# Kernel optimization log

Hardware: AMD Instinct MI355X
Metric: run time of the kernel (lower is better)

Reference implementation:

```python
import jax, jax.numpy as jnp
import numpy as np

D_M, D_K, D_V, HEADS = 1024, 64, 64, 16
B, S = 2, 2048


def setup_inputs() -> dict:
    key = jax.random.key(0)
    ks = jax.random.split(key, 5)
    x = jax.random.normal(ks[0], (B, S, D_M), dtype=jnp.float32)
    # per-head projection weights (original deep-copies one rand init per head;
    # we give each head independent weights, matching the per-head param structure)
    Wk = jax.random.uniform(ks[1], (HEADS, D_M, D_K), dtype=jnp.float32)
    Wq = jax.random.uniform(ks[2], (HEADS, D_M, D_K), dtype=jnp.float32)
    Wv = jax.random.uniform(ks[3], (HEADS, D_M, D_V), dtype=jnp.float32)
    Wo = jax.random.uniform(ks[4], (HEADS * D_V, D_M), dtype=jnp.float32)
    return {"x": x, "Wk": Wk, "Wq": Wq, "Wv": Wv, "Wo": Wo}


def reference(x, Wk, Wq, Wv, Wo):
    # per-head QKV projections, batched over heads: [B,H,S,d]
    q = jnp.einsum("bsm,hmk->bhsk", x, Wq)
    k = jnp.einsum("bsm,hmk->bhsk", x, Wk)
    v = jnp.einsum("bsm,hmv->bhsv", x, Wv)
    scale = 1.0 / jnp.sqrt(jnp.asarray(q.shape[-1], dtype=q.dtype))
    scores = jnp.einsum("bhsk,bhtk->bhst", q, k) * scale  # [B,H,S,S]
    attn = jax.nn.softmax(scores, axis=-1)
    ctx = jnp.einsum("bhst,bhtv->bhsv", attn, v)  # [B,H,S,d_v]
    # concat heads -> [B,S,H*d_v], then output projection
    ctx = jnp.transpose(ctx, (0, 2, 1, 3)).reshape(x.shape[0], x.shape[1], -1)
    return jnp.einsum("bsc,cm->bsm", ctx, Wo)
```

## Files before the change

### kernel.cpp

```cpp
#include <hip/hip_runtime.h>
#include <hip/hip_bf16.h>
#include <stdint.h>

#define DM   1024
#define DKV  64
#define HEADS 16
#define BATCH 2
#define SEQ  2048
#define BS   (BATCH*SEQ)
#define BHD  (BATCH*HEADS)

typedef __attribute__((ext_vector_type(8))) short bf16x8;
typedef __attribute__((ext_vector_type(4))) short bf16x4;
typedef __attribute__((ext_vector_type(4))) float f32x4;

__device__ inline unsigned short bf16_rtn(float f) {
  union { float f; unsigned u; } v; v.f = f;
  unsigned u = v.u;
  unsigned r = u + 0x7fffu + ((u >> 16) & 1u);
  return (unsigned short)(r >> 16);
}
__device__ inline float bf16_to_f(unsigned short h) {
  union { unsigned u; float f; } v; v.u = ((unsigned)h) << 16; return v.f;
}
__device__ inline void split_bf16(float x, unsigned short& hi, unsigned short& lo) {
  hi = bf16_rtn(x);
  lo = bf16_rtn(x - bf16_to_f(hi));
}

__device__ inline float fast_exp2(float x) {
#if __has_builtin(__builtin_amdgcn_exp2f)
  return __builtin_amdgcn_exp2f(x);
#else
  return exp2f(x);
#endif
}

__device__ inline f32x4 mfma16x16x16_bf16(bf16x4 a, bf16x4 b, f32x4 c) {
#if __has_builtin(__builtin_amdgcn_mfma_f32_16x16x16bf16_1k)
  return __builtin_amdgcn_mfma_f32_16x16x16bf16_1k(a, b, c, 0, 0, 0);
#else
  asm volatile("v_mfma_f32_16x16x16_bf16 %0, %1, %2, %0" : "+v"(c) : "v"(a), "v"(b));
  return c;
#endif
}

__device__ inline void stage16(const unsigned short* g, unsigned short* lds_base, int lane) {
#if __has_builtin(__builtin_amdgcn_global_load_lds)
  __builtin_amdgcn_global_load_lds((__attribute__((address_space(1))) void*)(g),
                                   (__attribute__((address_space(3))) void*)(lds_base),
                                   16, 0, 0);
#else
  *(bf16x8*)(lds_base + lane * 8) = *(const bf16x8*)g;
#endif
}

__global__ void cvt_x_split(const float* __restrict__ x,
                            unsigned short* __restrict__ xh, unsigned short* __restrict__ xl) {
  int i = (blockIdx.x * 256 + threadIdx.x) * 8;
  bf16x8 oh, ol;
  #pragma unroll
  for (int j = 0; j < 8; ++j) {
    unsigned short hi, lo;
    split_bf16(x[i + j], hi, lo);
    oh[j] = (short)hi; ol[j] = (short)lo;
  }
  *(bf16x8*)(xh + i) = oh;
  *(bf16x8*)(xl + i) = ol;
}

__global__ void pack_qkv_split(const float* __restrict__ Wq, const float* __restrict__ Wk,
                               const float* __restrict__ Wv,
                               unsigned short* __restrict__ Wh, unsigned short* __restrict__ Wl) {
  __shared__ float tile[64][65];
  int bid = blockIdx.x;
  int p = bid >> 8, h = (bid >> 4) & 15, mt = bid & 15;
  const float* W = (p == 0) ? Wq : (p == 1) ? Wk : Wv;
  const float* src = W + (size_t)h * (DM * DKV);
  int t = threadIdx.x;
  int m0 = mt * 64;
  #pragma unroll
  for (int pass = 0; pass < 16; ++pass) {
    int row = pass * 4 + (t >> 6), col = t & 63;
    tile[row][col] = src[(size_t)(m0 + row) * DKV + col];
  }
  __syncthreads();
  int cbase = p * 1024 + h * 64;
  #pragma unroll
  for (int pass = 0; pass < 16; ++pass) {
    int krow = pass * 4 + (t >> 6), mcol = t & 63;
    unsigned short hi, lo;
    split_bf16(tile[mcol][krow], hi, lo);
    size_t idx = (size_t)(cbase + krow) * DM + m0 + mcol;
    Wh[idx] = hi; Wl[idx] = lo;
  }
}

__global__ void pack_wo(const float* __restrict__ Wo, unsigned short* __restrict__ WoT) {
  __shared__ float tile[64][65];
  int ib = blockIdx.x >> 4, jb = blockIdx.x & 15;
  int t = threadIdx.x;
  #pragma unroll
  for (int pass = 0; pass < 16; ++pass) {
    int row = pass * 4 + (t >> 6), col = t & 63;
    tile[row][col] = Wo[(size_t)(ib * 64 + row) * DM + jb * 64 + col];
  }
  __syncthreads();
  #pragma unroll
  for (int pass = 0; pass < 16; ++pass) {
    int a = pass * 4 + (t >> 6), b = t & 63;
    WoT[(size_t)(jb * 64 + a) * DM + ib * 64 + b] = bf16_rtn(tile[b][a]);
  }
}

__global__ __launch_bounds__(256, 2)
void gemm1_split(const unsigned short* __restrict__ Ah, const unsigned short* __restrict__ Al,
                 const unsigned short* __restrict__ Bh, const unsigned short* __restrict__ Bl,
                 unsigned short* __restrict__ Qh, unsigned short* __restrict__ Ql,
                 unsigned short* __restrict__ Kh, unsigned short* __restrict__ Kl,
                 unsigned short* __restrict__ Vt) {
  __shared__ unsigned short AsH[128 * 32], AsL[128 * 32];
  __shared__ unsigned short BsH[128 * 32], BsL[128 * 32];
  const int tid = threadIdx.x;
  const int w = tid >> 6, lane = tid & 63;
  const int quad = lane >> 4, l16 = lane & 15;
  const int wm = w >> 1, wn = w & 1;
  const int bm = blockIdx.x, bn = blockIdx.y;

  f32x4 acc[4][4];
  #pragma unroll
  for (int i = 0; i < 4; ++i)
    #pragma unroll
    for (int j = 0; j < 4; ++j) acc[i][j] = (f32x4){0.f, 0.f, 0.f, 0.f};

  const int r4 = lane >> 2, c4 = lane & 3;
  const size_t offA = (size_t)(bm * 128 + w * 32 + r4) * DM + c4 * 8;
  const size_t offB = (size_t)(bn * 128 + w * 32 + r4) * DM + c4 * 8;
  unsigned short* lAh0 = AsH + (w * 32) * 32;      unsigned short* lAh1 = AsH + (w * 32 + 16) * 32;
  unsigned short* lAl0 = AsL + (w * 32) * 32;      unsigned short* lAl1 = AsL + (w * 32 + 16) * 32;
  unsigned short* lBh0 = BsH + (w * 32) * 32;      unsigned short* lBh1 = BsH + (w * 32 + 16) * 32;
  unsigned short* lBl0 = BsL + (w * 32) * 32;      unsigned short* lBl1 = BsL + (w * 32 + 16) * 32;

  for (int kk = 0; kk < DM / 32; ++kk) {
    stage16(Ah + offA + kk * 32,           lAh0, lane);
    stage16(Ah + offA + kk * 32 + 16 * DM, lAh1, lane);
    stage16(Al + offA + kk * 32,           lAl0, lane);
    stage16(Al + offA + kk * 32 + 16 * DM, lAl1, lane);
    stage16(Bh + offB + kk * 32,           lBh0, lane);
    stage16(Bh + offB + kk * 32 + 16 * DM, lBh1, lane);
    stage16(Bl + offB + kk * 32,           lBl0, lane);
    stage16(Bl + offB + kk * 32 + 16 * DM, lBl1, lane);
    asm volatile("s_waitcnt vmcnt(0)" ::: "memory");
    __syncthreads();
    bf16x8 afh[4], afl[4], bfh[4], bfl[4];
    #pragma unroll
    for (int mt = 0; mt < 4; ++mt) {
      afh[mt] = *(const bf16x8*)(AsH + (wm * 64 + mt * 16 + l16) * 32 + quad * 8);
      afl[mt] = *(const bf16x8*)(AsL + (wm * 64 + mt * 16 + l16) * 32 + quad * 8);
    }
    #pragma unroll
    for (int nt = 0; nt < 4; ++nt) {
      bfh[nt] = *(const bf16x8*)(BsH + (wn * 64 + nt * 16 + l16) * 32 + quad * 8);
      bfl[nt] = *(const bf16x8*)(BsL + (wn * 64 + nt * 16 + l16) * 32 + quad * 8);
    }
    #pragma unroll
    for (int mt = 0; mt < 4; ++mt)
      #pragma unroll
      for (int nt = 0; nt < 4; ++nt) {
        acc[mt][nt] = __builtin_amdgcn_mfma_f32_16x16x32_bf16(afh[mt], bfh[nt], acc[mt][nt], 0, 0, 0);
        acc[mt][nt] = __builtin_amdgcn_mfma_f32_16x16x32_bf16(afh[mt], bfl[nt], acc[mt][nt], 0, 0, 0);
        acc[mt][nt] = __builtin_amdgcn_mfma_f32_16x16x32_bf16(afl[mt], bfh[nt], acc[mt][nt], 0, 0, 0);
      }
    __syncthreads();
  }

  const float SCL = 0.18033688011112042f;
  #pragma unroll
  for (int mt = 0; mt < 4; ++mt) {
    int m_g = bm * 128 + wm * 64 + mt * 16 + quad * 4;
    #pragma unroll
    for (int nt = 0; nt < 4; ++nt) {
      int n_g = bn * 128 + wn * 64 + nt * 16 + l16;
      int p = n_g >> 10, h = (n_g >> 6) & 15, k = n_g & 63;
      #pragma unroll
      for (int r = 0; r < 4; ++r) {
        int row = m_g + r;
        int b = row >> 11, s = row & 2047;
        int bh = b * HEADS + h;
        float v = acc[mt][nt][r];
        if (p == 0) {
          unsigned short hi, lo; split_bf16(v * SCL, hi, lo);
          size_t idx = ((size_t)(bh * SEQ + s)) * DKV + k;
          Qh[idx] = hi; Ql[idx] = lo;
        } else if (p == 1) {
          unsigned short hi, lo; split_bf16(v, hi, lo);
          size_t idx = ((size_t)(bh * SEQ + s)) * DKV + k;
          Kh[idx] = hi; Kl[idx] = lo;
        } else {
          Vt[((size_t)(bh * DKV + k)) * SEQ + s] = bf16_rtn(v);
        }
      }
    }
  }
}

__global__ __launch_bounds__(256, 2)
void flash(const unsigned short* __restrict__ Qh, const unsigned short* __restrict__ Ql,
           const unsigned short* __restrict__ Kh, const unsigned short* __restrict__ Kl,
           const unsigned short* __restrict__ Vt, unsigned short* __restrict__ ctx) {
  __shared__ unsigned short KtH[64 * 72];
  __shared__ unsigned short KtL[64 * 72];
  __shared__ unsigned short Vts[64 * 72];
  const int tid = threadIdx.x;
  const int w = tid >> 6, lane = tid & 63, quad = lane >> 4, l16 = lane & 15;
  const int bh = blockIdx.y;
  const int q0 = blockIdx.x * 128;

  bf16x8 qfh[2][2], qfl[2][2];
  #pragma unroll
  for (int qt = 0; qt < 2; ++qt) {
    int qrow = q0 + w * 32 + qt * 16 + l16;
    size_t base = ((size_t)(bh * SEQ + qrow)) * DKV + quad * 8;
    qfh[qt][0] = *(const bf16x8*)(Qh + base);
    qfh[qt][1] = *(const bf16x8*)(Qh + base + 32);
    qfl[qt][0] = *(const bf16x8*)(Ql + base);
    qfl[qt][1] = *(const bf16x8*)(Ql + base + 32);
  }

  float m_run[2] = {-1e30f, -1e30f};
  float l_run[2] = {0.f, 0.f};
  f32x4 acc[2][4];
  #pragma unroll
  for (int qt = 0; qt < 2; ++qt)
    #pragma unroll
    for (int vt = 0; vt < 4; ++vt) acc[qt][vt] = (f32x4){0.f, 0.f, 0.f, 0.f};

  const int srow = tid >> 3, sc8 = tid & 7;

  for (int kt = 0; kt < SEQ / 64; ++kt) {
    int kt0 = kt * 64;
    #pragma unroll
    for (int pass = 0; pass < 2; ++pass) {
      int row = pass * 32 + srow;
      size_t kidx = ((size_t)(bh * SEQ + kt0 + row)) * DKV + sc8 * 8;
      *(bf16x8*)(KtH + row * 72 + sc8 * 8) = *(const bf16x8*)(Kh + kidx);
      *(bf16x8*)(KtL + row * 72 + sc8 * 8) = *(const bf16x8*)(Kl + kidx);
      *(bf16x8*)(Vts + row * 72 + sc8 * 8) =
          *(const bf16x8*)(Vt + ((size_t)(bh * DKV + row)) * SEQ + kt0 + sc8 * 8);
    }
    __syncthreads();

    f32x4 st[4][2];
    #pragma unroll
    for (int mt = 0; mt < 4; ++mt) {
      const unsigned short* kb = KtH + (mt * 16 + l16) * 72 + quad * 8;
      bf16x8 kah0 = *(const bf16x8*)(kb);
      bf16x8 kah1 = *(const bf16x8*)(kb + 32);
      const unsigned short* kbl = KtL + (mt * 16 + l16) * 72 + quad * 8;
      bf16x8 kal0 = *(const bf16x8*)(kbl);
      bf16x8 kal1 = *(const bf16x8*)(kbl + 32);
      #pragma unroll
      for (int qt = 0; qt < 2; ++qt) {
        f32x4 c = (f32x4){0.f, 0.f, 0.f, 0.f};
        c = __builtin_amdgcn_mfma_f32_16x16x32_bf16(kah0, qfh[qt][0], c, 0, 0, 0);
        c = __builtin_amdgcn_mfma_f32_16x16x32_bf16(kah1, qfh[qt][1], c, 0, 0, 0);
        c = __builtin_amdgcn_mfma_f32_16x16x32_bf16(kah0, qfl[qt][0], c, 0, 0, 0);
        c = __builtin_amdgcn_mfma_f32_16x16x32_bf16(kah1, qfl[qt][1], c, 0, 0, 0);
        c = __builtin_amdgcn_mfma_f32_16x16x32_bf16(kal0, qfh[qt][0], c, 0, 0, 0);
        c = __builtin_amdgcn_mfma_f32_16x16x32_bf16(kal1, qfh[qt][1], c, 0, 0, 0);
        st[mt][qt] = c;
      }
    }

    bf16x4 pb[2][4];
    #pragma unroll
    for (int qt = 0; qt < 2; ++qt) {
      float cm = -1e30f;
      #pragma unroll
      for (int mt = 0; mt < 4; ++mt)
        #pragma unroll
        for (int r = 0; r < 4; ++r) cm = fmaxf(cm, st[mt][qt][r]);
      cm = fmaxf(cm, __shfl_xor(cm, 16));
      cm = fmaxf(cm, __shfl_xor(cm, 32));
      float mn = fmaxf(m_run[qt], cm);
      float alpha = fast_exp2(m_run[qt] - mn);
      m_run[qt] = mn;
      float ssum = 0.f;
      #pragma unroll
      for (int mt = 0; mt < 4; ++mt) {
        bf16x4 pk;
        #pragma unroll
        for (int r = 0; r < 4; ++r) {
          float p = fast_exp2(st[mt][qt][r] - mn);
          ssum += p;
          pk[r] = (short)bf16_rtn(p);
        }
        pb[qt][mt] = pk;
      }
      ssum += __shfl_xor(ssum, 16);
      ssum += __shfl_xor(ssum, 32);
      l_run[qt] = l_run[qt] * alpha + ssum;
      #pragma unroll
      for (int vt = 0; vt < 4; ++vt) acc[qt][vt] = acc[qt][vt] * alpha;
    }

    #pragma unroll
    for (int vt = 0; vt < 4; ++vt) {
      #pragma unroll
      for (int mt = 0; mt < 4; ++mt) {
        bf16x4 va = *(const bf16x4*)(Vts + (vt * 16 + l16) * 72 + mt * 16 + quad * 4);
        #pragma unroll
        for (int qt = 0; qt < 2; ++qt)
          acc[qt][vt] = mfma16x16x16_bf16(va, pb[qt][mt], acc[qt][vt]);
      }
    }
    __syncthreads();
  }

  int h = bh & 15, b = bh >> 4;
  #pragma unroll
  for (int qt = 0; qt < 2; ++qt) {
    float inv = 1.0f / l_run[qt];
    int bs = b * SEQ + q0 + w * 32 + qt * 16 + l16;
    #pragma unroll
    for (int vt = 0; vt < 4; ++vt)
      #pragma unroll
      for (int r = 0; r < 4; ++r)
        ctx[(size_t)bs * DM + h * 64 + vt * 16 + quad * 4 + r] = bf16_rtn(acc[qt][vt][r] * inv);
  }
}

__global__ __launch_bounds__(256, 2)
void gemm_out(const unsigned short* __restrict__ A, const unsigned short* __restrict__ Bt,
              float* __restrict__ out) {
  __shared__ unsigned short As[128 * 32];
  __shared__ unsigned short Bs[128 * 32];
  const int tid = threadIdx.x;
  const int w = tid >> 6, lane = tid & 63;
  const int quad = lane >> 4, l16 = lane & 15;
  const int wm = w >> 1, wn = w & 1;
  const int bm = blockIdx.x, bn = blockIdx.y;

  f32x4 acc[4][4];
  #pragma unroll
  for (int i = 0; i < 4; ++i)
    #pragma unroll
    for (int j = 0; j < 4; ++j) acc[i][j] = (f32x4){0.f, 0.f, 0.f, 0.f};

  const int r4 = lane >> 2, c4 = lane & 3;
  const unsigned short* gA0 = A  + (size_t)(bm * 128 + w * 32 + r4) * DM + c4 * 8;
  const unsigned short* gB0 = Bt + (size_t)(bn * 128 + w * 32 + r4) * DM + c4 * 8;
  unsigned short* lA0 = As + (w * 32) * 32;
  unsigned short* lA1 = As + (w * 32 + 16) * 32;
  unsigned short* lB0 = Bs + (w * 32) * 32;
  unsigned short* lB1 = Bs + (w * 32 + 16) * 32;

  for (int kk = 0; kk < DM / 32; ++kk) {
    stage16(gA0 + kk * 32,           lA0, lane);
    stage16(gA0 + kk * 32 + 16 * DM, lA1, lane);
    stage16(gB0 + kk * 32,           lB0, lane);
    stage16(gB0 + kk * 32 + 16 * DM, lB1, lane);
    asm volatile("s_waitcnt vmcnt(0)" ::: "memory");
    __syncthreads();
    bf16x8 af[4], bfr[4];
    #pragma unroll
    for (int mt = 0; mt < 4; ++mt)
      af[mt] = *(const bf16x8*)(As + (wm * 64 + mt * 16 + l16) * 32 + quad * 8);
    #pragma unroll
    for (int nt = 0; nt < 4; ++nt)
      bfr[nt] = *(const bf16x8*)(Bs + (wn * 64 + nt * 16 + l16) * 32 + quad * 8);
    #pragma unroll
    for (int mt = 0; mt < 4; ++mt)
      #pragma unroll
      for (int nt = 0; nt < 4; ++nt)
        acc[mt][nt] = __builtin_amdgcn_mfma_f32_16x16x32_bf16(af[mt], bfr[nt], acc[mt][nt], 0, 0, 0);
    __syncthreads();
  }

  #pragma unroll
  for (int mt = 0; mt < 4; ++mt) {
    int m_g = bm * 128 + wm * 64 + mt * 16 + quad * 4;
    #pragma unroll
    for (int nt = 0; nt < 4; ++nt) {
      int n_g = bn * 128 + wn * 64 + nt * 16 + l16;
      #pragma unroll
      for (int r = 0; r < 4; ++r)
        out[(size_t)(m_g + r) * DM + n_g] = acc[mt][nt][r];
    }
  }
}

extern "C" void kernel_launch(void* const* d_in, const int* in_sizes, int n_in,
                              void* d_out, int out_size, void* d_ws, size_t ws_size,
                              hipStream_t stream) {
  const float* x  = (const float*)d_in[0];
  const float* Wk = (const float*)d_in[1];
  const float* Wq = (const float*)d_in[2];
  const float* Wv = (const float*)d_in[3];
  const float* Wo = (const float*)d_in[4];
  float* out = (float*)d_out;

  unsigned short* xh  = (unsigned short*)d_ws;
  unsigned short* xl  = xh  + (size_t)BS * DM;
  unsigned short* Wh  = xl  + (size_t)BS * DM;
  unsigned short* Wl  = Wh  + (size_t)3 * DM * DM;
  unsigned short* WoT = Wl  + (size_t)3 * DM * DM;
  unsigned short* Qh  = WoT + (size_t)DM * DM;
  unsigned short* Ql  = Qh  + (size_t)BHD * SEQ * DKV;
  unsigned short* Kh  = Ql  + (size_t)BHD * SEQ * DKV;
  unsigned short* Kl  = Kh  + (size_t)BHD * SEQ * DKV;
  unsigned short* Vtb = Kl  + (size_t)BHD * SEQ * DKV;
  unsigned short* ctx = Vtb + (size_t)BHD * SEQ * DKV;

  cvt_x_split<<<(BS * DM) / (256 * 8), 256, 0, stream>>>(x, xh, xl);
  pack_qkv_split<<<3 * 16 * 16, 256, 0, stream>>>(Wq, Wk, Wv, Wh, Wl);
  pack_wo<<<16 * 16, 256, 0, stream>>>(Wo, WoT);
  gemm1_split<<<dim3(BS / 128, 3072 / 128), 256, 0, stream>>>(xh, xl, Wh, Wl, Qh, Ql, Kh, Kl, Vtb);
  flash<<<dim3(SEQ / 128, BHD), 256, 0, stream>>>(Qh, Ql, Kh, Kl, Vtb, ctx);
  gemm_out<<<dim3(BS / 128, DM / 128), 256, 0, stream>>>(ctx, WoT, out);
}
```

Measured before the change: 280.9 us.

## Split V projection into single-pass GEMM and pipeline flash K/V loads with swizzled LDS

The fused QKV split-bf16 GEMM becomes two kernels. Q and K keep the hi/lo split GEMM, while V uses a cheaper single bf16 GEMM because it is rounded to bf16 anyway. The flash kernel prefetches the next K/V tile into registers while computing the current one, and replaces padded LDS rows with an XOR swizzle. It also skips the accumulator rescale when no row max changes and packs bf16 conversions with perm, giving vectorized ctx stores. Grid dimensions are swapped for all GEMMs and flash to change block scheduling order, at the cost of more register pressure from the prefetch buffers.

```diff
diff --git a/kernel.cpp b/kernel.cpp
--- a/kernel.cpp
+++ b/kernel.cpp
@@ -14,9 +14,10 @@
 typedef __attribute__((ext_vector_type(4))) short bf16x4;
 typedef __attribute__((ext_vector_type(4))) float f32x4;
 
+__device__ inline unsigned fb(float f) { union { float f; unsigned u; } v; v.f = f; return v.u; }
+
 __device__ inline unsigned short bf16_rtn(float f) {
-  union { float f; unsigned u; } v; v.f = f;
-  unsigned u = v.u;
+  unsigned u = fb(f);
   unsigned r = u + 0x7fffu + ((u >> 16) & 1u);
   return (unsigned short)(r >> 16);
 }
@@ -26,6 +27,9 @@
 __device__ inline void split_bf16(float x, unsigned short& hi, unsigned short& lo) {
   hi = bf16_rtn(x);
   lo = bf16_rtn(x - bf16_to_f(hi));
+}
+__device__ inline unsigned pack2_bf16(float lo_elem, float hi_elem) {
+  return __builtin_amdgcn_perm(fb(hi_elem) + 0x8000u, fb(lo_elem) + 0x8000u, 0x07060302u);
 }
 
 __device__ inline float fast_exp2(float x) {
@@ -53,6 +57,10 @@
 #else
   *(bf16x8*)(lds_base + lane * 8) = *(const bf16x8*)g;
 #endif
+}
+
+__device__ inline int swz(int row, int chunk) {
+  return row * 64 + (((chunk ^ (row & 7)) & 7) << 3);
 }
 
 __global__ void cvt_x_split(const float* __restrict__ x,
@@ -114,18 +122,17 @@
 }
 
 __global__ __launch_bounds__(256, 2)
-void gemm1_split(const unsigned short* __restrict__ Ah, const unsigned short* __restrict__ Al,
-                 const unsigned short* __restrict__ Bh, const unsigned short* __restrict__ Bl,
-                 unsigned short* __restrict__ Qh, unsigned short* __restrict__ Ql,
-                 unsigned short* __restrict__ Kh, unsigned short* __restrict__ Kl,
-                 unsigned short* __restrict__ Vt) {
+void gemm_qk(const unsigned short* __restrict__ Ah, const unsigned short* __restrict__ Al,
+             const unsigned short* __restrict__ Bh, const unsigned short* __restrict__ Bl,
+             unsigned short* __restrict__ Qh, unsigned short* __restrict__ Ql,
+             unsigned short* __restrict__ Kh, unsigned short* __restrict__ Kl) {
   __shared__ unsigned short AsH[128 * 32], AsL[128 * 32];
   __shared__ unsigned short BsH[128 * 32], BsL[128 * 32];
   const int tid = threadIdx.x;
   const int w = tid >> 6, lane = tid & 63;
   const int quad = lane >> 4, l16 = lane & 15;
   const int wm = w >> 1, wn = w & 1;
-  const int bm = blockIdx.x, bn = blockIdx.y;
+  const int bn = blockIdx.x, bm = blockIdx.y;
 
   f32x4 acc[4][4];
   #pragma unroll
@@ -188,17 +195,80 @@
         int b = row >> 11, s = row & 2047;
         int bh = b * HEADS + h;
         float v = acc[mt][nt][r];
+        size_t idx = ((size_t)(bh * SEQ + s)) * DKV + k;
+        unsigned short hi, lo;
         if (p == 0) {
-          unsigned short hi, lo; split_bf16(v * SCL, hi, lo);
-          size_t idx = ((size_t)(bh * SEQ + s)) * DKV + k;
+          split_bf16(v * SCL, hi, lo);
           Qh[idx] = hi; Ql[idx] = lo;
-        } else if (p == 1) {
-          unsigned short hi, lo; split_bf16(v, hi, lo);
-          size_t idx = ((size_t)(bh * SEQ + s)) * DKV + k;
+        } else {
+          split_bf16(v, hi, lo);
           Kh[idx] = hi; Kl[idx] = lo;
-        } else {
-          Vt[((size_t)(bh * DKV + k)) * SEQ + s] = bf16_rtn(v);
         }
+      }
+    }
+  }
+}
+
+__global__ __launch_bounds__(256, 2)
+void gemm_v(const unsigned short* __restrict__ A, const unsigned short* __restrict__ Bt,
+            unsigned short* __restrict__ Vt) {
+  __shared__ unsigned short As[128 * 32];
+  __shared__ unsigned short Bs[128 * 32];
+  const int tid = threadIdx.x;
+  const int w = tid >> 6, lane = tid & 63;
+  const int quad = lane >> 4, l16 = lane & 15;
+  const int wm = w >> 1, wn = w & 1;
+  const int bn = blockIdx.x, bm = blockIdx.y;
+
+  f32x4 acc[4][4];
+  #pragma unroll
+  for (int i = 0; i < 4; ++i)
+    #pragma unroll
+    for (int j = 0; j < 4; ++j) acc[i][j] = (f32x4){0.f, 0.f, 0.f, 0.f};
+
+  const int r4 = lane >> 2, c4 = lane & 3;
+  const unsigned short* gA0 = A  + (size_t)(bm * 128 + w * 32 + r4) * DM + c4 * 8;
+  const unsigned short* gB0 = Bt + (size_t)(bn * 128 + w * 32 + r4) * DM + c4 * 8;
+  unsigned short* lA0 = As + (w * 32) * 32;
+  unsigned short* lA1 = As + (w * 32 + 16) * 32;
+  unsigned short* lB0 = Bs + (w * 32) * 32;
+  unsigned short* lB1 = Bs + (w * 32 + 16) * 32;
+
+  for (int kk = 0; kk < DM / 32; ++kk) {
+    stage16(gA0 + kk * 32,           lA0, lane);
+    stage16(gA0 + kk * 32 + 16 * DM, lA1, lane);
+    stage16(gB0 + kk * 32,           lB0, lane);
+    stage16(gB0 + kk * 32 + 16 * DM, lB1, lane);
+    asm volatile("s_waitcnt vmcnt(0)" ::: "memory");
+    __syncthreads();
+    bf16x8 af[4], bfr[4];
+    #pragma unroll
+    for (int mt = 0; mt < 4; ++mt)
+      af[mt] = *(const bf16x8*)(As + (wm * 64 + mt * 16 + l16) * 32 + quad * 8);
+    #pragma unroll
+    for (int nt = 0; nt < 4; ++nt)
+      bfr[nt] = *(const bf16x8*)(Bs + (wn * 64 + nt * 16 + l16) * 32 + quad * 8);
+    #pragma unroll
+    for (int mt = 0; mt < 4; ++mt)
+      #pragma unroll
+      for (int nt = 0; nt < 4; ++nt)
+        acc[mt][nt] = __builtin_amdgcn_mfma_f32_16x16x32_bf16(af[mt], bfr[nt], acc[mt][nt], 0, 0, 0);
+    __syncthreads();
+  }
+
+  #pragma unroll
+  for (int mt = 0; mt < 4; ++mt) {
+    int m_g = bm * 128 + wm * 64 + mt * 16 + quad * 4;
+    #pragma unroll
+    for (int nt = 0; nt < 4; ++nt) {
+      int n_g = bn * 128 + wn * 64 + nt * 16 + l16;
+      int h = n_g >> 6, k = n_g & 63;
+      #pragma unroll
+      for (int r = 0; r < 4; ++r) {
+        int row = m_g + r;
+        int b = row >> 11, s = row & 2047;
+        int bh = b * HEADS + h;
+        Vt[((size_t)(bh * DKV + k)) * SEQ + s] = bf16_rtn(acc[mt][nt][r]);
       }
     }
   }
@@ -208,13 +278,11 @@
 void flash(const unsigned short* __restrict__ Qh, const unsigned short* __restrict__ Ql,
            const unsigned short* __restrict__ Kh, const unsigned short* __restrict__ Kl,
            const unsigned short* __restrict__ Vt, unsigned short* __restrict__ ctx) {
-  __shared__ unsigned short KtH[64 * 72];
-  __shared__ unsigned short KtL[64 * 72];
-  __shared__ unsigned short Vts[64 * 72];
+  __shared__ unsigned short KtH[64 * 64], KtL[64 * 64], Vts[64 * 64];
   const int tid = threadIdx.x;
   const int w = tid >> 6, lane = tid & 63, quad = lane >> 4, l16 = lane & 15;
-  const int bh = blockIdx.y;
-  const int q0 = blockIdx.x * 128;
+  const int bh = blockIdx.x;
+  const int q0 = blockIdx.y * 128;
 
   bf16x8 qfh[2][2], qfl[2][2];
   #pragma unroll
@@ -237,28 +305,47 @@
 
   const int srow = tid >> 3, sc8 = tid & 7;
 
+  bf16x8 rkh[2], rkl[2], rv[2];
+  #pragma unroll
+  for (int p = 0; p < 2; ++p) {
+    int row = p * 32 + srow;
+    size_t kidx = ((size_t)(bh * SEQ + row)) * DKV + sc8 * 8;
+    rkh[p] = *(const bf16x8*)(Kh + kidx);
+    rkl[p] = *(const bf16x8*)(Kl + kidx);
+    rv[p]  = *(const bf16x8*)(Vt + ((size_t)(bh * DKV + row)) * SEQ + sc8 * 8);
+  }
+
   for (int kt = 0; kt < SEQ / 64; ++kt) {
-    int kt0 = kt * 64;
-    #pragma unroll
-    for (int pass = 0; pass < 2; ++pass) {
-      int row = pass * 32 + srow;
-      size_t kidx = ((size_t)(bh * SEQ + kt0 + row)) * DKV + sc8 * 8;
-      *(bf16x8*)(KtH + row * 72 + sc8 * 8) = *(const bf16x8*)(Kh + kidx);
-      *(bf16x8*)(KtL + row * 72 + sc8 * 8) = *(const bf16x8*)(Kl + kidx);
-      *(bf16x8*)(Vts + row * 72 + sc8 * 8) =
-          *(const bf16x8*)(Vt + ((size_t)(bh * DKV + row)) * SEQ + kt0 + sc8 * 8);
-    }
-    __syncthreads();
+    __syncthreads();
+    #pragma unroll
+    for (int p = 0; p < 2; ++p) {
+      int row = p * 32 + srow;
+      int o = swz(row, sc8);
+      *(bf16x8*)(KtH + o) = rkh[p];
+      *(bf16x8*)(KtL + o) = rkl[p];
+      *(bf16x8*)(Vts + o) = rv[p];
+    }
+    __syncthreads();
+    if (kt + 1 < SEQ / 64) {
+      int kt0 = (kt + 1) * 64;
+      #pragma unroll
+      for (int p = 0; p < 2; ++p) {
+        int row = p * 32 + srow;
+        size_t kidx = ((size_t)(bh * SEQ + kt0 + row)) * DKV + sc8 * 8;
+        rkh[p] = *(const bf16x8*)(Kh + kidx);
+        rkl[p] = *(const bf16x8*)(Kl + kidx);
+        rv[p]  = *(const bf16x8*)(Vt + ((size_t)(bh * DKV + row)) * SEQ + kt0 + sc8 * 8);
+      }
+    }
 
     f32x4 st[4][2];
     #pragma unroll
     for (int mt = 0; mt < 4; ++mt) {
-      const unsigned short* kb = KtH + (mt * 16 + l16) * 72 + quad * 8;
-      bf16x8 kah0 = *(const bf16x8*)(kb);
-      bf16x8 kah1 = *(const bf16x8*)(kb + 32);
-      const unsigned short* kbl = KtL + (mt * 16 + l16) * 72 + quad * 8;
-      bf16x8 kal0 = *(const bf16x8*)(kbl);
-      bf16x8 kal1 = *(const bf16x8*)(kbl + 32);
+      int rowA = mt * 16 + l16;
+      bf16x8 kah0 = *(const bf16x8*)(KtH + swz(rowA, quad));
+      bf16x8 kah1 = *(const bf16x8*)(KtH + swz(rowA, quad + 4));
+      bf16x8 kal0 = *(const bf16x8*)(KtL + swz(rowA, quad));
+      bf16x8 kal1 = *(const bf16x8*)(KtL + swz(rowA, quad + 4));
       #pragma unroll
       for (int qt = 0; qt < 2; ++qt) {
         f32x4 c = (f32x4){0.f, 0.f, 0.f, 0.f};
@@ -282,39 +369,46 @@
         for (int r = 0; r < 4; ++r) cm = fmaxf(cm, st[mt][qt][r]);
       cm = fmaxf(cm, __shfl_xor(cm, 16));
       cm = fmaxf(cm, __shfl_xor(cm, 32));
-      float mn = fmaxf(m_run[qt], cm);
-      float alpha = fast_exp2(m_run[qt] - mn);
-      m_run[qt] = mn;
+      bool upd = cm > m_run[qt];
+      float mn = upd ? cm : m_run[qt];
       float ssum = 0.f;
       #pragma unroll
       for (int mt = 0; mt < 4; ++mt) {
-        bf16x4 pk;
-        #pragma unroll
-        for (int r = 0; r < 4; ++r) {
-          float p = fast_exp2(st[mt][qt][r] - mn);
-          ssum += p;
-          pk[r] = (short)bf16_rtn(p);
-        }
-        pb[qt][mt] = pk;
+        float p0 = fast_exp2(st[mt][qt][0] - mn);
+        float p1 = fast_exp2(st[mt][qt][1] - mn);
+        float p2 = fast_exp2(st[mt][qt][2] - mn);
+        float p3 = fast_exp2(st[mt][qt][3] - mn);
+        ssum += (p0 + p1) + (p2 + p3);
+        union { bf16x4 v; unsigned u2[2]; } pk;
+        pk.u2[0] = pack2_bf16(p0, p1);
+        pk.u2[1] = pack2_bf16(p2, p3);
+        pb[qt][mt] = pk.v;
       }
       ssum += __shfl_xor(ssum, 16);
       ssum += __shfl_xor(ssum, 32);
-      l_run[qt] = l_run[qt] * alpha + ssum;
-      #pragma unroll
-      for (int vt = 0; vt < 4; ++vt) acc[qt][vt] = acc[qt][vt] * alpha;
+      if (__ballot(upd)) {
+        float alpha = fast_exp2(m_run[qt] - mn);
+        m_run[qt] = mn;
+        l_run[qt] = l_run[qt] * alpha + ssum;
+        #pragma unroll
+        for (int vt = 0; vt < 4; ++vt) acc[qt][vt] = acc[qt][vt] * alpha;
+      } else {
+        l_run[qt] += ssum;
+      }
     }
 
     #pragma unroll
     for (int vt = 0; vt < 4; ++vt) {
       #pragma unroll
       for (int mt = 0; mt < 4; ++mt) {
-        bf16x4 va = *(const bf16x4*)(Vts + (vt * 16 + l16) * 72 + mt * 16 + quad * 4);
+        int row = vt * 16 + l16;
+        int addr = row * 64 + ((((mt * 2 + (quad >> 1)) ^ (row & 7)) & 7) << 3) + (quad & 1) * 4;
+        bf16x4 va = *(const bf16x4*)(Vts + addr);
         #pragma unroll
         for (int qt = 0; qt < 2; ++qt)
           acc[qt][vt] = mfma16x16x16_bf16(va, pb[qt][mt], acc[qt][vt]);
       }
     }
-    __syncthreads();
   }
 
   int h = bh & 15, b = bh >> 4;
@@ -323,10 +417,12 @@
     float inv = 1.0f / l_run[qt];
     int bs = b * SEQ + q0 + w * 32 + qt * 16 + l16;
     #pragma unroll
-    for (int vt = 0; vt < 4; ++vt)
-      #pragma unroll
-      for (int r = 0; r < 4; ++r)
-        ctx[(size_t)bs * DM + h * 64 + vt * 16 + quad * 4 + r] = bf16_rtn(acc[qt][vt][r] * inv);
+    for (int vt = 0; vt < 4; ++vt) {
+      union { bf16x4 v; unsigned u2[2]; } pk;
+      pk.u2[0] = pack2_bf16(acc[qt][vt][0] * inv, acc[qt][vt][1] * inv);
+      pk.u2[1] = pack2_bf16(acc[qt][vt][2] * inv, acc[qt][vt][3] * inv);
+      *(bf16x4*)(ctx + (size_t)bs * DM + h * 64 + vt * 16 + quad * 4) = pk.v;
+    }
   }
 }
 
@@ -339,7 +435,7 @@
   const int w = tid >> 6, lane = tid & 63;
   const int quad = lane >> 4, l16 = lane & 15;
   const int wm = w >> 1, wn = w & 1;
-  const int bm = blockIdx.x, bn = blockIdx.y;
+  const int bn = blockIdx.x, bm = blockIdx.y;
 
   f32x4 acc[4][4];
   #pragma unroll
@@ -415,7 +511,8 @@
   cvt_x_split<<<(BS * DM) / (256 * 8), 256, 0, stream>>>(x, xh, xl);
   pack_qkv_split<<<3 * 16 * 16, 256, 0, stream>>>(Wq, Wk, Wv, Wh, Wl);
   pack_wo<<<16 * 16, 256, 0, stream>>>(Wo, WoT);
-  gemm1_split<<<dim3(BS / 128, 3072 / 128), 256, 0, stream>>>(xh, xl, Wh, Wl, Qh, Ql, Kh, Kl, Vtb);
-  flash<<<dim3(SEQ / 128, BHD), 256, 0, stream>>>(Qh, Ql, Kh, Kl, Vtb, ctx);
-  gemm_out<<<dim3(BS / 128, DM / 128), 256, 0, stream>>>(ctx, WoT, out);
-}
+  gemm_qk<<<dim3(16, 32), 256, 0, stream>>>(xh, xl, Wh, Wl, Qh, Ql, Kh, Kl);
+  gemm_v<<<dim3(8, 32), 256, 0, stream>>>(xh, Wh + (size_t)2048 * DM, Vtb);
+  flash<<<dim3(BHD, SEQ / 128), 256, 0, stream>>>(Qh, Ql, Kh, Kl, Vtb, ctx);
+  gemm_out<<<dim3(8, 32), 256, 0, stream>>>(ctx, WoT, out);
+}
```

New measurement: 270.8 us. 1.04x faster.
